# Kernel optimization log

Hardware: AMD Instinct MI355X
Metric: run time of the kernel (lower is better)

Reference implementation:

```python
import jax, jax.numpy as jnp
import numpy as np


def setup_inputs() -> dict:
    key = jax.random.key(0)
    k1, k2 = jax.random.split(key)
    B, H, S, Dh = 2, 16, 2048, 64
    x1 = jax.random.normal(k1, (B, H, S, S), dtype=jnp.float32)   # attention scores
    x2 = jax.random.normal(k2, (B, H, Dh, S), dtype=jnp.float32)  # will be transposed to [B,H,S,Dh]
    return {"x1": x1, "x2": x2}


def reference(x1, x2):
    # F.softmax(x1, dim=-1).matmul(x2.transpose(-2, -1))
    # The Masker/sparsify in the original forward only packs activations for the
    # approximate backward pass; it does not change the forward output.
    sm = jax.nn.softmax(x1, axis=-1)                      # [B,H,Sq,Sk]
    out = jnp.einsum('bhqk,bhdk->bhqd', sm, x2)           # sm @ x2^T -> [B,H,Sq,Dh]
    return out
```

## Files before the change

kernel.cpp:

```cpp
#include <hip/hip_runtime.h>
#include <math.h>

typedef _Float16 f16x8 __attribute__((ext_vector_type(8)));
typedef float    f32x4 __attribute__((ext_vector_type(4)));

#define SEQ   2048
#define DH    64
#define BM    64
#define BK    64
#define LOG2E 1.44269504088896340736f

extern "C" __global__ __launch_bounds__(256, 4)
void softmax_matmul_f16(const float* __restrict__ x1,
                        const float* __restrict__ x2,
                        float* __restrict__ out)
{
    const int tid  = threadIdx.x;
    const int wave = tid >> 6;
    const int lane = tid & 63;
    const int r    = lane & 15;
    const int quad = lane >> 4;

    const int bh   = blockIdx.x >> 5;
    const int qblk = blockIdx.x & 31;
    const int row0 = qblk * BM + wave * 16;

    const float* x1row = x1 + ((size_t)bh * SEQ + (size_t)(row0 + r)) * SEQ;
    const float* x2bh  = x2 + (size_t)bh * DH * SEQ;
    float*       obase = out + ((size_t)bh * SEQ + (size_t)row0) * DH;

    f32x4 acc[4];
#pragma unroll
    for (int t = 0; t < 4; ++t) acc[t] = (f32x4){0.f, 0.f, 0.f, 0.f};

    float m = -INFINITY;
    float l = 0.0f;

    const float* pf = x1row + quad * 8;
    float4 n0 = *(const float4*)(pf + 0);
    float4 n1 = *(const float4*)(pf + 4);
    float4 n2 = *(const float4*)(pf + 32);
    float4 n3 = *(const float4*)(pf + 36);

    for (int k0 = 0; k0 < SEQ; k0 += BK) {
        float xv[16];
        xv[0] = n0.x; xv[1] = n0.y; xv[2]  = n0.z; xv[3]  = n0.w;
        xv[4] = n1.x; xv[5] = n1.y; xv[6]  = n1.z; xv[7]  = n1.w;
        xv[8] = n2.x; xv[9] = n2.y; xv[10] = n2.z; xv[11] = n2.w;
        xv[12] = n3.x; xv[13] = n3.y; xv[14] = n3.z; xv[15] = n3.w;

        const int k1 = k0 + BK;
        if (k1 < SEQ) {
            const float* pn = x1row + k1 + quad * 8;
            n0 = *(const float4*)(pn + 0);
            n1 = *(const float4*)(pn + 4);
            n2 = *(const float4*)(pn + 32);
            n3 = *(const float4*)(pn + 36);
        }

        float cmax = xv[0];
#pragma unroll
        for (int j = 1; j < 16; ++j) cmax = fmaxf(cmax, xv[j]);
        cmax = fmaxf(cmax, __shfl_xor(cmax, 16));
        cmax = fmaxf(cmax, __shfl_xor(cmax, 32));

        const float mnew  = fmaxf(m, cmax);
        const float alpha = __builtin_amdgcn_exp2f((m - mnew) * LOG2E);
        const float sh    = mnew * LOG2E;

        float p[16];
        float rsum = 0.f;
#pragma unroll
        for (int j = 0; j < 16; ++j) {
            p[j] = __builtin_amdgcn_exp2f(__builtin_fmaf(xv[j], LOG2E, -sh));
            rsum += p[j];
        }
        rsum += __shfl_xor(rsum, 16);
        rsum += __shfl_xor(rsum, 32);
        l = l * alpha + rsum;
        m = mnew;

        float ar[4];
#pragma unroll
        for (int g = 0; g < 4; ++g) ar[g] = __shfl(alpha, quad * 4 + g);
#pragma unroll
        for (int t = 0; t < 4; ++t)
#pragma unroll
            for (int g = 0; g < 4; ++g) acc[t][g] *= ar[g];

        f16x8 ah0, ah1;
#pragma unroll
        for (int j = 0; j < 8; ++j) {
            ah0[j] = (_Float16)p[j];
            ah1[j] = (_Float16)p[8 + j];
        }

#pragma unroll
        for (int t = 0; t < 4; ++t) {
            const float* bp = x2bh + (size_t)(t * 16 + r) * SEQ + k0 + quad * 8;
            float4 b0 = *(const float4*)(bp + 0);
            float4 b1 = *(const float4*)(bp + 4);
            float4 b2 = *(const float4*)(bp + 32);
            float4 b3 = *(const float4*)(bp + 36);
            f16x8 bf0, bf1;
            bf0[0] = (_Float16)b0.x; bf0[1] = (_Float16)b0.y; bf0[2] = (_Float16)b0.z; bf0[3] = (_Float16)b0.w;
            bf0[4] = (_Float16)b1.x; bf0[5] = (_Float16)b1.y; bf0[6] = (_Float16)b1.z; bf0[7] = (_Float16)b1.w;
            bf1[0] = (_Float16)b2.x; bf1[1] = (_Float16)b2.y; bf1[2] = (_Float16)b2.z; bf1[3] = (_Float16)b2.w;
            bf1[4] = (_Float16)b3.x; bf1[5] = (_Float16)b3.y; bf1[6] = (_Float16)b3.z; bf1[7] = (_Float16)b3.w;
            acc[t] = __builtin_amdgcn_mfma_f32_16x16x32_f16(ah0, bf0, acc[t], 0, 0, 0);
            acc[t] = __builtin_amdgcn_mfma_f32_16x16x32_f16(ah1, bf1, acc[t], 0, 0, 0);
        }
    }

    const float rl = 1.0f / l;
    float rlr[4];
#pragma unroll
    for (int g = 0; g < 4; ++g) rlr[g] = __shfl(rl, quad * 4 + g);
#pragma unroll
    for (int t = 0; t < 4; ++t)
#pragma unroll
        for (int g = 0; g < 4; ++g)
            obase[(size_t)(quad * 4 + g) * DH + t * 16 + r] = acc[t][g] * rlr[g];
}

extern "C" void kernel_launch(void* const* d_in, const int* in_sizes, int n_in,
                              void* d_out, int out_size, void* d_ws, size_t ws_size,
                              hipStream_t stream)
{
    const float* x1 = (const float*)d_in[0];
    const float* x2 = (const float*)d_in[1];
    float* out = (float*)d_out;

    const int bhCount = in_sizes[1] / (DH * SEQ);
    dim3 grid(bhCount * (SEQ / BM));
    dim3 block(256);
    hipLaunchKernelGGL(softmax_matmul_f16, grid, block, 0, stream, x1, x2, out);
}
```

Baseline: 839.0 us.

## Pre-convert x2 to fp16 and stage coalesced x1 rows through LDS

```diff
diff --git a/kernel.cpp b/kernel.cpp
--- a/kernel.cpp
+++ b/kernel.cpp
@@ -2,19 +2,34 @@
 #include <math.h>
 
 typedef _Float16 f16x8 __attribute__((ext_vector_type(8)));
+typedef _Float16 f16x4 __attribute__((ext_vector_type(4)));
 typedef float    f32x4 __attribute__((ext_vector_type(4)));
 
 #define SEQ   2048
 #define DH    64
 #define BM    64
 #define BK    64
+#define LDSW  68
 #define LOG2E 1.44269504088896340736f
+
+extern "C" __global__ __launch_bounds__(256)
+void cvt_x2_f16(const float* __restrict__ x2, _Float16* __restrict__ y)
+{
+    size_t i = ((size_t)blockIdx.x * 256 + threadIdx.x) * 4;
+    float4 v = *(const float4*)(x2 + i);
+    f16x4 h;
+    h[0] = (_Float16)v.x; h[1] = (_Float16)v.y;
+    h[2] = (_Float16)v.z; h[3] = (_Float16)v.w;
+    *(f16x4*)(y + i) = h;
+}
 
 extern "C" __global__ __launch_bounds__(256, 4)
 void softmax_matmul_f16(const float* __restrict__ x1,
-                        const float* __restrict__ x2,
+                        const _Float16* __restrict__ x2h,
                         float* __restrict__ out)
 {
+    __shared__ __align__(16) float lds[4][2][16][LDSW];
+
     const int tid  = threadIdx.x;
     const int wave = tid >> 6;
     const int lane = tid & 63;
@@ -25,9 +40,11 @@
     const int qblk = blockIdx.x & 31;
     const int row0 = qblk * BM + wave * 16;
 
-    const float* x1row = x1 + ((size_t)bh * SEQ + (size_t)(row0 + r)) * SEQ;
-    const float* x2bh  = x2 + (size_t)bh * DH * SEQ;
-    float*       obase = out + ((size_t)bh * SEQ + (size_t)row0) * DH;
+    const float*    x1w  = x1  + ((size_t)bh * SEQ + row0) * SEQ;
+    const _Float16* x2b  = x2h + (size_t)bh * DH * SEQ;
+    float*          obase = out + ((size_t)bh * SEQ + row0) * DH;
+
+    const int lc = (lane & 15) * 4;
 
     f32x4 acc[4];
 #pragma unroll
@@ -36,27 +53,43 @@
     float m = -INFINITY;
     float l = 0.0f;
 
-    const float* pf = x1row + quad * 8;
-    float4 n0 = *(const float4*)(pf + 0);
-    float4 n1 = *(const float4*)(pf + 4);
-    float4 n2 = *(const float4*)(pf + 32);
-    float4 n3 = *(const float4*)(pf + 36);
+    float4 g[4];
+#pragma unroll
+    for (int i = 0; i < 4; ++i)
+        g[i] = *(const float4*)(x1w + (size_t)(i * 4 + quad) * SEQ + lc);
 
+    int buf = 0;
     for (int k0 = 0; k0 < SEQ; k0 += BK) {
-        float xv[16];
-        xv[0] = n0.x; xv[1] = n0.y; xv[2]  = n0.z; xv[3]  = n0.w;
-        xv[4] = n1.x; xv[5] = n1.y; xv[6]  = n1.z; xv[7]  = n1.w;
-        xv[8] = n2.x; xv[9] = n2.y; xv[10] = n2.z; xv[11] = n2.w;
-        xv[12] = n3.x; xv[13] = n3.y; xv[14] = n3.z; xv[15] = n3.w;
+#pragma unroll
+        for (int i = 0; i < 4; ++i)
+            *(float4*)&lds[wave][buf][i * 4 + quad][lc] = g[i];
 
         const int k1 = k0 + BK;
         if (k1 < SEQ) {
-            const float* pn = x1row + k1 + quad * 8;
-            n0 = *(const float4*)(pn + 0);
-            n1 = *(const float4*)(pn + 4);
-            n2 = *(const float4*)(pn + 32);
-            n3 = *(const float4*)(pn + 36);
+#pragma unroll
+            for (int i = 0; i < 4; ++i)
+                g[i] = *(const float4*)(x1w + (size_t)(i * 4 + quad) * SEQ + k1 + lc);
         }
+
+        f16x8 bf[8];
+#pragma unroll
+        for (int t = 0; t < 4; ++t) {
+            const _Float16* bp = x2b + (size_t)(t * 16 + r) * SEQ + k0 + quad * 8;
+            bf[2 * t]     = *(const f16x8*)bp;
+            bf[2 * t + 1] = *(const f16x8*)(bp + 32);
+        }
+
+        float4 a0 = *(const float4*)&lds[wave][buf][r][quad * 8];
+        float4 a1 = *(const float4*)&lds[wave][buf][r][quad * 8 + 4];
+        float4 a2 = *(const float4*)&lds[wave][buf][r][32 + quad * 8];
+        float4 a3 = *(const float4*)&lds[wave][buf][r][36 + quad * 8];
+        buf ^= 1;
+
+        float xv[16];
+        xv[0]  = a0.x; xv[1]  = a0.y; xv[2]  = a0.z; xv[3]  = a0.w;
+        xv[4]  = a1.x; xv[5]  = a1.y; xv[6]  = a1.z; xv[7]  = a1.w;
+        xv[8]  = a2.x; xv[9]  = a2.y; xv[10] = a2.z; xv[11] = a2.w;
+        xv[12] = a3.x; xv[13] = a3.y; xv[14] = a3.z; xv[15] = a3.w;
 
         float cmax = xv[0];
 #pragma unroll
@@ -82,11 +115,11 @@
 
         float ar[4];
 #pragma unroll
-        for (int g = 0; g < 4; ++g) ar[g] = __shfl(alpha, quad * 4 + g);
+        for (int gi = 0; gi < 4; ++gi) ar[gi] = __shfl(alpha, quad * 4 + gi);
 #pragma unroll
         for (int t = 0; t < 4; ++t)
 #pragma unroll
-            for (int g = 0; g < 4; ++g) acc[t][g] *= ar[g];
+            for (int gi = 0; gi < 4; ++gi) acc[t][gi] *= ar[gi];
 
         f16x8 ah0, ah1;
 #pragma unroll
@@ -97,30 +130,20 @@
 
 #pragma unroll
         for (int t = 0; t < 4; ++t) {
-            const float* bp = x2bh + (size_t)(t * 16 + r) * SEQ + k0 + quad * 8;
-            float4 b0 = *(const float4*)(bp + 0);
-            float4 b1 = *(const float4*)(bp + 4);
-            float4 b2 = *(const float4*)(bp + 32);
-            float4 b3 = *(const float4*)(bp + 36);
-            f16x8 bf0, bf1;
-            bf0[0] = (_Float16)b0.x; bf0[1] = (_Float16)b0.y; bf0[2] = (_Float16)b0.z; bf0[3] = (_Float16)b0.w;
-            bf0[4] = (_Float16)b1.x; bf0[5] = (_Float16)b1.y; bf0[6] = (_Float16)b1.z; bf0[7] = (_Float16)b1.w;
-            bf1[0] = (_Float16)b2.x; bf1[1] = (_Float16)b2.y; bf1[2] = (_Float16)b2.z; bf1[3] = (_Float16)b2.w;
-            bf1[4] = (_Float16)b3.x; bf1[5] = (_Float16)b3.y; bf1[6] = (_Float16)b3.z; bf1[7] = (_Float16)b3.w;
-            acc[t] = __builtin_amdgcn_mfma_f32_16x16x32_f16(ah0, bf0, acc[t], 0, 0, 0);
-            acc[t] = __builtin_amdgcn_mfma_f32_16x16x32_f16(ah1, bf1, acc[t], 0, 0, 0);
+            acc[t] = __builtin_amdgcn_mfma_f32_16x16x32_f16(ah0, bf[2 * t],     acc[t], 0, 0, 0);
+            acc[t] = __builtin_amdgcn_mfma_f32_16x16x32_f16(ah1, bf[2 * t + 1], acc[t], 0, 0, 0);
         }
     }
 
     const float rl = 1.0f / l;
     float rlr[4];
 #pragma unroll
-    for (int g = 0; g < 4; ++g) rlr[g] = __shfl(rl, quad * 4 + g);
+    for (int gi = 0; gi < 4; ++gi) rlr[gi] = __shfl(rl, quad * 4 + gi);
 #pragma unroll
     for (int t = 0; t < 4; ++t)
 #pragma unroll
-        for (int g = 0; g < 4; ++g)
-            obase[(size_t)(quad * 4 + g) * DH + t * 16 + r] = acc[t][g] * rlr[g];
+        for (int gi = 0; gi < 4; ++gi)
+            obase[(size_t)(quad * 4 + gi) * DH + t * 16 + r] = acc[t][gi] * rlr[gi];
 }
 
 extern "C" void kernel_launch(void* const* d_in, const int* in_sizes, int n_in,
@@ -130,9 +153,12 @@
     const float* x1 = (const float*)d_in[0];
     const float* x2 = (const float*)d_in[1];
     float* out = (float*)d_out;
+    _Float16* x2h = (_Float16*)d_ws;
 
     const int bhCount = in_sizes[1] / (DH * SEQ);
-    dim3 grid(bhCount * (SEQ / BM));
-    dim3 block(256);
-    hipLaunchKernelGGL(softmax_matmul_f16, grid, block, 0, stream, x1, x2, out);
+    const int nEl     = in_sizes[1];
+
+    hipLaunchKernelGGL(cvt_x2_f16, dim3(nEl / (256 * 4)), dim3(256), 0, stream, x2, x2h);
+    hipLaunchKernelGGL(softmax_matmul_f16, dim3(bhCount * (SEQ / BM)), dim3(256), 0, stream,
+                       x1, x2h, out);
 }
```

New measurement: 840.9 us. Within noise of the previous version (+0.2%).
